# Optimization experiments

Hardware: AMD Instinct MI355X
Metric: run time of the kernel (lower is better)

## Reference

```python
import jax, jax.numpy as jnp
import numpy as np

NEG_SLOPE = 0.2  # GATConv default negative_slope

def setup_inputs() -> dict:
    key = jax.random.key(0)
    k1, k2, k3, k4 = jax.random.split(key, 4)
    N, Cin, Cout = 2048, 128, 64
    return {
        "data": jax.random.normal(k1, (N, Cin), jnp.float32),
        "W": jax.random.normal(k2, (Cin, Cout), jnp.float32) / np.sqrt(Cin).astype(np.float32),
        "att_src": jax.random.normal(k3, (Cout,), jnp.float32) * 0.1,
        "att_dst": jax.random.normal(k4, (Cout,), jnp.float32) * 0.1,
        "bias": jnp.zeros((Cout,), jnp.float32),
    }

def reference(data, W, att_src, att_dst, bias):
    N = data.shape[0]
    # torch.combinations(arange(N)).t(): edges (i, j) with i < j, src=i, dst=j
    rows, cols = jnp.triu_indices(N, k=1)
    loop = jnp.arange(N)  # GATConv add_self_loops=True
    src = jnp.concatenate([rows, loop])
    dst = jnp.concatenate([cols, loop])

    h = data @ W                       # [N, Cout]
    a_s = h @ att_src                  # [N]
    a_d = h @ att_dst                  # [N]

    # per-edge attention logits, leaky_relu, segment softmax over dst
    e = jax.nn.leaky_relu(a_s[src] + a_d[dst], NEG_SLOPE)          # [E]
    m = jax.ops.segment_max(e, dst, num_segments=N)                # [N]
    ex = jnp.exp(e - m[dst])                                       # [E]
    denom = jax.ops.segment_sum(ex, dst, num_segments=N)           # [N]
    alpha = ex / denom[dst]                                        # [E]

    # scatter-add weighted source features
    out = jax.ops.segment_sum(alpha[:, None] * h[src], dst, num_segments=N) + bias
    return jax.nn.relu(out)
```

## Files before the change

### kernel.cpp

```cpp
#include <hip/hip_runtime.h>
#include <hip/hip_bf16.h>
#include <math.h>

#define N 2048
#define CIN 128
#define COUT 64
#define NEG 0.2f
#define JB 16
#define NJB (N / JB)

typedef __attribute__((ext_vector_type(8))) short short8;
typedef __attribute__((ext_vector_type(4))) float f32x4;

__device__ __forceinline__ ushort bf16u(float x) {
  __hip_bfloat16 b = __float2bfloat16(x);
  return *reinterpret_cast<ushort*>(&b);
}
__device__ __forceinline__ uint pack2(float lo, float hi) {
  return (uint)bf16u(lo) | ((uint)bf16u(hi) << 16);
}

__global__ __launch_bounds__(256) void gat_gemm_mfma(
    const float* __restrict__ data, const float* __restrict__ W,
    const float* __restrict__ att_src, const float* __restrict__ att_dst,
    ushort* __restrict__ hfrag, float* __restrict__ a_s,
    float* __restrict__ a_d) {
  const int tid = (int)threadIdx.x;
  const int ci = tid >> 6;
  const int lane = tid & 63;
  const int i0 = (int)blockIdx.x * 16;
  const int q = lane >> 4;
  const int n15 = lane & 15;
  const int mrow = i0 + n15;

  short8 af[4];
#pragma unroll
  for (int kc = 0; kc < 4; ++kc) {
    const int col = kc * 32 + q * 8;
    const float4 f0 = *(const float4*)&data[mrow * CIN + col];
    const float4 f1 = *(const float4*)&data[mrow * CIN + col + 4];
    uint4 pa;
    pa.x = pack2(f0.x, f0.y);
    pa.y = pack2(f0.z, f0.w);
    pa.z = pack2(f1.x, f1.y);
    pa.w = pack2(f1.z, f1.w);
    af[kc] = *(short8*)&pa;
  }

  const int cg = ci * 16 + n15;
  f32x4 acc = {0.f, 0.f, 0.f, 0.f};
#pragma unroll
  for (int kc = 0; kc < 4; ++kc) {
    const int kr = kc * 32 + q * 8;
    ushort uw[8];
#pragma unroll
    for (int e = 0; e < 8; ++e) uw[e] = bf16u(W[(kr + e) * COUT + cg]);
    uint4 pw;
    pw.x = (uint)uw[0] | ((uint)uw[1] << 16);
    pw.y = (uint)uw[2] | ((uint)uw[3] << 16);
    pw.z = (uint)uw[4] | ((uint)uw[5] << 16);
    pw.w = (uint)uw[6] | ((uint)uw[7] << 16);
    acc = __builtin_amdgcn_mfma_f32_16x16x32_bf16(af[kc], *(short8*)&pw,
                                                  acc, 0, 0, 0);
  }

  {
    const int ib = i0 + q * 4;
    const int f = (ib >> 5) * 4 + ci;
    const int lp = ((ib >> 3) & 3) * 16 + n15;
    uint2 hv;
    hv.x = pack2(acc[0], acc[1]);
    hv.y = pack2(acc[2], acc[3]);
    *(uint2*)&hfrag[((size_t)(f * 64 + lp) << 3) + (ib & 7)] = hv;
  }

  __shared__ float asp[4][16];
  __shared__ float adp[4][16];
  {
    const float sc = att_src[cg];
    const float dc = att_dst[cg];
    float ps[4], pd[4];
#pragma unroll
    for (int r = 0; r < 4; ++r) { ps[r] = acc[r] * sc; pd[r] = acc[r] * dc; }
#pragma unroll
    for (int off = 1; off < 16; off <<= 1) {
#pragma unroll
      for (int r = 0; r < 4; ++r) {
        ps[r] += __shfl_xor(ps[r], off);
        pd[r] += __shfl_xor(pd[r], off);
      }
    }
    if (n15 == 0) {
#pragma unroll
      for (int r = 0; r < 4; ++r) {
        asp[ci][q * 4 + r] = ps[r];
        adp[ci][q * 4 + r] = pd[r];
      }
    }
  }
  __syncthreads();
  if (tid < 16) {
    a_s[i0 + tid] = asp[0][tid] + asp[1][tid] + asp[2][tid] + asp[3][tid];
    a_d[i0 + tid] = adp[0][tid] + adp[1][tid] + adp[2][tid] + adp[3][tid];
  }
}

__global__ __launch_bounds__(1024) void gat_attn_flash(
    const ushort* __restrict__ hfrag, const float* __restrict__ a_s,
    const float* __restrict__ a_d, const float* __restrict__ bias,
    float* __restrict__ out) {
  const int bj = NJB - 1 - (int)blockIdx.x;
  const int tid = (int)threadIdx.x;
  const int wid = tid >> 6;
  const int lane = tid & 63;
  const int j0 = bj * JB;
  const int jme = j0 + (lane & 15);
  const int kgrp = lane >> 4;
  const float ad_me = a_d[jme];
  const int nks = (bj + 2) >> 1;

  f32x4 acc0 = {0.f, 0.f, 0.f, 0.f};
  f32x4 acc1 = acc0, acc2 = acc0, acc3 = acc0;
  float dsum = 0.f;
  const uint4* hf = (const uint4*)hfrag;

  for (int ks = wid; ks < nks; ks += 16) {
    const int ibase = ks * 32 + kgrp * 8;
    const float4 asa = *(const float4*)&a_s[ibase];
    const float4 asb = *(const float4*)&a_s[ibase + 4];
    const float av[8] = {asa.x, asa.y, asa.z, asa.w,
                         asb.x, asb.y, asb.z, asb.w};
    short8 af;
#pragma unroll
    for (int e = 0; e < 8; ++e) {
      float x = av[e] + ad_me;
      x = fmaxf(x, NEG * x);
      float wgt = __expf(x);
      if (ibase + e > jme) wgt = 0.f;
      dsum += wgt;
      af[e] = (short)bf16u(wgt);
    }
    const int fbase = (ks * 4) * 64 + lane;
    const uint4 b0 = hf[fbase];
    const uint4 b1 = hf[fbase + 64];
    const uint4 b2 = hf[fbase + 128];
    const uint4 b3 = hf[fbase + 192];
    acc0 = __builtin_amdgcn_mfma_f32_16x16x32_bf16(af, *(const short8*)&b0,
                                                   acc0, 0, 0, 0);
    acc1 = __builtin_amdgcn_mfma_f32_16x16x32_bf16(af, *(const short8*)&b1,
                                                   acc1, 0, 0, 0);
    acc2 = __builtin_amdgcn_mfma_f32_16x16x32_bf16(af, *(const short8*)&b2,
                                                   acc2, 0, 0, 0);
    acc3 = __builtin_amdgcn_mfma_f32_16x16x32_bf16(af, *(const short8*)&b3,
                                                   acc3, 0, 0, 0);
  }

  dsum += __shfl_xor(dsum, 16);
  dsum += __shfl_xor(dsum, 32);

  __shared__ float rbuf[16][16][64];
  __shared__ float dbuf[16][16];
#pragma unroll
  for (int r = 0; r < 4; ++r) {
    rbuf[0 + r][wid][lane]  = acc0[r];
    rbuf[4 + r][wid][lane]  = acc1[r];
    rbuf[8 + r][wid][lane]  = acc2[r];
    rbuf[12 + r][wid][lane] = acc3[r];
  }
  if (lane < 16) dbuf[wid][lane] = dsum;
  __syncthreads();

  {
    const int j = tid >> 6, c = tid & 63;
    const int qq = j >> 2, rr = j & 3, t16 = c >> 4, n = c & 15;
    float num = 0.f, den = 0.f;
#pragma unroll
    for (int ww = 0; ww < 16; ++ww) {
      num += rbuf[t16 * 4 + rr][ww][qq * 16 + n];
      den += dbuf[ww][j];
    }
    const float v = num / den + bias[c];
    out[(size_t)(j0 + j) * COUT + c] = v > 0.f ? v : 0.f;
  }
}

extern "C" void kernel_launch(void* const* d_in, const int* in_sizes, int n_in,
                              void* d_out, int out_size, void* d_ws, size_t ws_size,
                              hipStream_t stream) {
  const float* data    = (const float*)d_in[0];
  const float* W       = (const float*)d_in[1];
  const float* att_src = (const float*)d_in[2];
  const float* att_dst = (const float*)d_in[3];
  const float* bias    = (const float*)d_in[4];
  float* out = (float*)d_out;

  ushort* hfrag = (ushort*)d_ws;
  float* a_s  = (float*)d_ws + 65536;
  float* a_d  = a_s + N;

  gat_gemm_mfma<<<N / 16, 256, 0, stream>>>(data, W, att_src, att_dst,
                                            hfrag, a_s, a_d);
  gat_attn_flash<<<NJB, 1024, 0, stream>>>(hfrag, a_s, a_d, bias, out);
}
```

Measured before the change: 15.11 us.

## Fuse projection GEMM into attention kernel, recomputing h panels per block

```diff
diff --git a/kernel.cpp b/kernel.cpp
--- a/kernel.cpp
+++ b/kernel.cpp
@@ -20,38 +20,33 @@
   return (uint)bf16u(lo) | ((uint)bf16u(hi) << 16);
 }
 
-__global__ __launch_bounds__(256) void gat_gemm_mfma(
+__global__ __launch_bounds__(1024) void gat_fused(
     const float* __restrict__ data, const float* __restrict__ W,
     const float* __restrict__ att_src, const float* __restrict__ att_dst,
-    ushort* __restrict__ hfrag, float* __restrict__ a_s,
-    float* __restrict__ a_d) {
+    const float* __restrict__ bias, float* __restrict__ out) {
+  const int bj = NJB - 1 - (int)blockIdx.x;
   const int tid = (int)threadIdx.x;
-  const int ci = tid >> 6;
+  const int wid = tid >> 6;
   const int lane = tid & 63;
-  const int i0 = (int)blockIdx.x * 16;
   const int q = lane >> 4;
   const int n15 = lane & 15;
-  const int mrow = i0 + n15;
-
-  short8 af[4];
-#pragma unroll
-  for (int kc = 0; kc < 4; ++kc) {
-    const int col = kc * 32 + q * 8;
-    const float4 f0 = *(const float4*)&data[mrow * CIN + col];
-    const float4 f1 = *(const float4*)&data[mrow * CIN + col + 4];
-    uint4 pa;
-    pa.x = pack2(f0.x, f0.y);
-    pa.y = pack2(f0.z, f0.w);
-    pa.z = pack2(f1.x, f1.y);
-    pa.w = pack2(f1.z, f1.w);
-    af[kc] = *(short8*)&pa;
-  }
-
-  const int cg = ci * 16 + n15;
-  f32x4 acc = {0.f, 0.f, 0.f, 0.f};
-#pragma unroll
-  for (int kc = 0; kc < 4; ++kc) {
-    const int kr = kc * 32 + q * 8;
+  const int j0 = bj * JB;
+  const int jme = j0 + n15;
+  const int nks = (bj + 2) >> 1;
+
+  __shared__ char smem[16384 + 16 * 4096];
+  __shared__ float asbuf[16][32];
+  __shared__ float adbuf[16];
+  __shared__ float dbuf[16][16];
+  ushort* wbuf = (ushort*)smem;
+  ushort* hw = (ushort*)(smem + 16384 + wid * 4096);
+  float* rbuf = (float*)smem;
+
+  {
+    const int kc = tid >> 8, L = tid & 63;
+    const int ci = (tid >> 6) & 3;
+    const int kr = kc * 32 + (L >> 4) * 8;
+    const int cg = ci * 16 + (L & 15);
     ushort uw[8];
 #pragma unroll
     for (int e = 0; e < 8; ++e) uw[e] = bf16u(W[(kr + e) * COUT + cg]);
@@ -60,74 +55,112 @@
     pw.y = (uint)uw[2] | ((uint)uw[3] << 16);
     pw.z = (uint)uw[4] | ((uint)uw[5] << 16);
     pw.w = (uint)uw[6] | ((uint)uw[7] << 16);
-    acc = __builtin_amdgcn_mfma_f32_16x16x32_bf16(af[kc], *(short8*)&pw,
-                                                  acc, 0, 0, 0);
-  }
-
-  {
-    const int ib = i0 + q * 4;
-    const int f = (ib >> 5) * 4 + ci;
-    const int lp = ((ib >> 3) & 3) * 16 + n15;
-    uint2 hv;
-    hv.x = pack2(acc[0], acc[1]);
-    hv.y = pack2(acc[2], acc[3]);
-    *(uint2*)&hfrag[((size_t)(f * 64 + lp) << 3) + (ib & 7)] = hv;
-  }
-
-  __shared__ float asp[4][16];
-  __shared__ float adp[4][16];
-  {
-    const float sc = att_src[cg];
-    const float dc = att_dst[cg];
-    float ps[4], pd[4];
-#pragma unroll
-    for (int r = 0; r < 4; ++r) { ps[r] = acc[r] * sc; pd[r] = acc[r] * dc; }
-#pragma unroll
-    for (int off = 1; off < 16; off <<= 1) {
-#pragma unroll
-      for (int r = 0; r < 4; ++r) {
-        ps[r] += __shfl_xor(ps[r], off);
-        pd[r] += __shfl_xor(pd[r], off);
-      }
-    }
+    *(uint4*)&wbuf[tid * 8] = pw;
+  }
+
+  float srcv[4], dstv[4];
+#pragma unroll
+  for (int ci = 0; ci < 4; ++ci) {
+    srcv[ci] = att_src[ci * 16 + n15];
+    dstv[ci] = att_dst[ci * 16 + n15];
+  }
+  __syncthreads();
+
+  f32x4 pacc0 = {0.f, 0.f, 0.f, 0.f};
+  f32x4 pacc1 = pacc0, pacc2 = pacc0, pacc3 = pacc0;
+  float dsum = 0.f;
+  float ad_me = 0.f;
+
+  const int nt = (wid < nks) ? ((nks - 1 - wid) >> 4) + 1 : 0;
+  const int w0 = (nks - 1) & 15;
+  const int t_first = (wid == w0) ? ((nks - 1 - wid) >> 4) : 0;
+
+  auto gen_panel = [&](int ks, bool do_ad) {
+    const int ibase = ks * 32;
+    f32x4 acc[2][4];
+#pragma unroll
+    for (int mi = 0; mi < 2; ++mi)
+#pragma unroll
+      for (int ci = 0; ci < 4; ++ci) acc[mi][ci] = (f32x4){0.f, 0.f, 0.f, 0.f};
+
+#pragma unroll
+    for (int kc = 0; kc < 4; ++kc) {
+      short8 af[2];
+#pragma unroll
+      for (int mi = 0; mi < 2; ++mi) {
+        const int mrow = ibase + mi * 16 + n15;
+        const int col = kc * 32 + q * 8;
+        const float4 f0 = *(const float4*)&data[mrow * CIN + col];
+        const float4 f1 = *(const float4*)&data[mrow * CIN + col + 4];
+        uint4 pa;
+        pa.x = pack2(f0.x, f0.y);
+        pa.y = pack2(f0.z, f0.w);
+        pa.z = pack2(f1.x, f1.y);
+        pa.w = pack2(f1.z, f1.w);
+        af[mi] = *(short8*)&pa;
+      }
+#pragma unroll
+      for (int ci = 0; ci < 4; ++ci) {
+        const short8 bw =
+            *(const short8*)&wbuf[((kc * 4 + ci) * 64 + lane) * 8];
+        acc[0][ci] = __builtin_amdgcn_mfma_f32_16x16x32_bf16(af[0], bw,
+                                                             acc[0][ci], 0, 0, 0);
+        acc[1][ci] = __builtin_amdgcn_mfma_f32_16x16x32_bf16(af[1], bw,
+                                                             acc[1][ci], 0, 0, 0);
+      }
+    }
+
+    float ps[2][4] = {};
+    float pd[2][4] = {};
+#pragma unroll
+    for (int mi = 0; mi < 2; ++mi) {
+      const int ibl = mi * 16 + q * 4;
+      const int lp = ((ibl >> 3) & 3) * 16 + n15;
+#pragma unroll
+      for (int ci = 0; ci < 4; ++ci) {
+        uint2 hv;
+        hv.x = pack2(acc[mi][ci][0], acc[mi][ci][1]);
+        hv.y = pack2(acc[mi][ci][2], acc[mi][ci][3]);
+        *(uint2*)&hw[(ci * 64 + lp) * 8 + (ibl & 7)] = hv;
+#pragma unroll
+        for (int r = 0; r < 4; ++r) {
+          ps[mi][r] = fmaf(acc[mi][ci][r], srcv[ci], ps[mi][r]);
+          if (do_ad) pd[mi][r] = fmaf(acc[mi][ci][r], dstv[ci], pd[mi][r]);
+        }
+      }
+    }
+#pragma unroll
+    for (int off = 1; off < 16; off <<= 1)
+#pragma unroll
+      for (int mi = 0; mi < 2; ++mi)
+#pragma unroll
+        for (int r = 0; r < 4; ++r) ps[mi][r] += __shfl_xor(ps[mi][r], off);
     if (n15 == 0) {
 #pragma unroll
-      for (int r = 0; r < 4; ++r) {
-        asp[ci][q * 4 + r] = ps[r];
-        adp[ci][q * 4 + r] = pd[r];
-      }
-    }
-  }
-  __syncthreads();
-  if (tid < 16) {
-    a_s[i0 + tid] = asp[0][tid] + asp[1][tid] + asp[2][tid] + asp[3][tid];
-    a_d[i0 + tid] = adp[0][tid] + adp[1][tid] + adp[2][tid] + adp[3][tid];
-  }
-}
-
-__global__ __launch_bounds__(1024) void gat_attn_flash(
-    const ushort* __restrict__ hfrag, const float* __restrict__ a_s,
-    const float* __restrict__ a_d, const float* __restrict__ bias,
-    float* __restrict__ out) {
-  const int bj = NJB - 1 - (int)blockIdx.x;
-  const int tid = (int)threadIdx.x;
-  const int wid = tid >> 6;
-  const int lane = tid & 63;
-  const int j0 = bj * JB;
-  const int jme = j0 + (lane & 15);
-  const int kgrp = lane >> 4;
-  const float ad_me = a_d[jme];
-  const int nks = (bj + 2) >> 1;
-
-  f32x4 acc0 = {0.f, 0.f, 0.f, 0.f};
-  f32x4 acc1 = acc0, acc2 = acc0, acc3 = acc0;
-  float dsum = 0.f;
-  const uint4* hf = (const uint4*)hfrag;
-
-  for (int ks = wid; ks < nks; ks += 16) {
-    const int ibase = ks * 32 + kgrp * 8;
-    const float4 asa = *(const float4*)&a_s[ibase];
-    const float4 asb = *(const float4*)&a_s[ibase + 4];
+      for (int mi = 0; mi < 2; ++mi)
+#pragma unroll
+        for (int r = 0; r < 4; ++r) asbuf[wid][mi * 16 + q * 4 + r] = ps[mi][r];
+    }
+    if (do_ad) {
+#pragma unroll
+      for (int off = 1; off < 16; off <<= 1)
+#pragma unroll
+        for (int mi = 0; mi < 2; ++mi)
+#pragma unroll
+          for (int r = 0; r < 4; ++r) pd[mi][r] += __shfl_xor(pd[mi][r], off);
+      if (n15 == 0) {
+        const int msel = bj & 1;
+#pragma unroll
+        for (int r = 0; r < 4; ++r)
+          adbuf[q * 4 + r] = msel ? pd[1][r] : pd[0][r];
+      }
+    }
+  };
+
+  auto consume = [&](int ks) {
+    const int ibase = ks * 32;
+    const float4 asa = *(const float4*)&asbuf[wid][q * 8];
+    const float4 asb = *(const float4*)&asbuf[wid][q * 8 + 4];
     const float av[8] = {asa.x, asa.y, asa.z, asa.w,
                          asb.x, asb.y, asb.z, asb.w};
     short8 af;
@@ -136,36 +169,43 @@
       float x = av[e] + ad_me;
       x = fmaxf(x, NEG * x);
       float wgt = __expf(x);
-      if (ibase + e > jme) wgt = 0.f;
+      if (ibase + q * 8 + e > jme) wgt = 0.f;
       dsum += wgt;
       af[e] = (short)bf16u(wgt);
     }
-    const int fbase = (ks * 4) * 64 + lane;
-    const uint4 b0 = hf[fbase];
-    const uint4 b1 = hf[fbase + 64];
-    const uint4 b2 = hf[fbase + 128];
-    const uint4 b3 = hf[fbase + 192];
-    acc0 = __builtin_amdgcn_mfma_f32_16x16x32_bf16(af, *(const short8*)&b0,
-                                                   acc0, 0, 0, 0);
-    acc1 = __builtin_amdgcn_mfma_f32_16x16x32_bf16(af, *(const short8*)&b1,
-                                                   acc1, 0, 0, 0);
-    acc2 = __builtin_amdgcn_mfma_f32_16x16x32_bf16(af, *(const short8*)&b2,
-                                                   acc2, 0, 0, 0);
-    acc3 = __builtin_amdgcn_mfma_f32_16x16x32_bf16(af, *(const short8*)&b3,
-                                                   acc3, 0, 0, 0);
+    const short8 b0 = *(const short8*)&hw[(0 * 64 + lane) * 8];
+    const short8 b1 = *(const short8*)&hw[(1 * 64 + lane) * 8];
+    const short8 b2 = *(const short8*)&hw[(2 * 64 + lane) * 8];
+    const short8 b3 = *(const short8*)&hw[(3 * 64 + lane) * 8];
+    pacc0 = __builtin_amdgcn_mfma_f32_16x16x32_bf16(af, b0, pacc0, 0, 0, 0);
+    pacc1 = __builtin_amdgcn_mfma_f32_16x16x32_bf16(af, b1, pacc1, 0, 0, 0);
+    pacc2 = __builtin_amdgcn_mfma_f32_16x16x32_bf16(af, b2, pacc2, 0, 0, 0);
+    pacc3 = __builtin_amdgcn_mfma_f32_16x16x32_bf16(af, b3, pacc3, 0, 0, 0);
+  };
+
+  if (nt > 0) gen_panel(wid + 16 * t_first, wid == w0);
+  __syncthreads();
+  ad_me = adbuf[n15];
+  if (nt > 0) consume(wid + 16 * t_first);
+
+#pragma unroll 1
+  for (int t = 0; t < nt; ++t) {
+    if (t == t_first) continue;
+    const int ks = wid + 16 * t;
+    gen_panel(ks, false);
+    consume(ks);
   }
 
   dsum += __shfl_xor(dsum, 16);
   dsum += __shfl_xor(dsum, 32);
 
-  __shared__ float rbuf[16][16][64];
-  __shared__ float dbuf[16][16];
+  __syncthreads();
 #pragma unroll
   for (int r = 0; r < 4; ++r) {
-    rbuf[0 + r][wid][lane]  = acc0[r];
-    rbuf[4 + r][wid][lane]  = acc1[r];
-    rbuf[8 + r][wid][lane]  = acc2[r];
-    rbuf[12 + r][wid][lane] = acc3[r];
+    rbuf[((0 + r) * 16 + wid) * 64 + lane]  = pacc0[r];
+    rbuf[((4 + r) * 16 + wid) * 64 + lane]  = pacc1[r];
+    rbuf[((8 + r) * 16 + wid) * 64 + lane]  = pacc2[r];
+    rbuf[((12 + r) * 16 + wid) * 64 + lane] = pacc3[r];
   }
   if (lane < 16) dbuf[wid][lane] = dsum;
   __syncthreads();
@@ -176,7 +216,7 @@
     float num = 0.f, den = 0.f;
 #pragma unroll
     for (int ww = 0; ww < 16; ++ww) {
-      num += rbuf[t16 * 4 + rr][ww][qq * 16 + n];
+      num += rbuf[((t16 * 4 + rr) * 16 + ww) * 64 + qq * 16 + n];
       den += dbuf[ww][j];
     }
     const float v = num / den + bias[c];
@@ -194,11 +234,5 @@
   const float* bias    = (const float*)d_in[4];
   float* out = (float*)d_out;
 
-  ushort* hfrag = (ushort*)d_ws;
-  float* a_s  = (float*)d_ws + 65536;
-  float* a_d  = a_s + N;
-
-  gat_gemm_mfma<<<N / 16, 256, 0, stream>>>(data, W, att_src, att_dst,
-                                            hfrag, a_s, a_d);
-  gat_attn_flash<<<NJB, 1024, 0, stream>>>(hfrag, a_s, a_d, bias, out);
-}
+  gat_fused<<<NJB, 1024, 0, stream>>>(data, W, att_src, att_dst, bias, out);
+}
```

Result: slower. 44.87 us (+196.9%).
